# Kernel tuning notes

Hardware: AMD Instinct MI355X
Metric: run time of the kernel (lower is better)

The kernel has to match this reference:

```python
import jax, jax.numpy as jnp
import numpy as np

LEVELS = [(128, 128), (64, 64), (32, 32), (16, 16)]  # (h, w) per level
NUM_HEADS = 8
NUM_LEVELS = 4
NUM_POINTS = 4
EMBED_DIMS = 256


def _bilinear_sample(img, gx, gy):
    """grid_sample(mode='bilinear', padding_mode='zeros', align_corners=False).
    img: (B, H, W, C); gx, gy: (B, N) in [-1, 1]. Returns (B, N, C)."""
    B, H, W, C = img.shape
    x = ((gx + 1.0) * W - 1.0) * 0.5
    y = ((gy + 1.0) * H - 1.0) * 0.5
    x0 = jnp.floor(x)
    y0 = jnp.floor(y)
    wx1 = x - x0
    wy1 = y - y0
    flat = img.reshape(B, H * W, C)

    def gather(xf, yf, w):
        xi = xf.astype(jnp.int32)
        yi = yf.astype(jnp.int32)
        valid = (xi >= 0) & (xi < W) & (yi >= 0) & (yi < H)
        idx = jnp.clip(yi, 0, H - 1) * W + jnp.clip(xi, 0, W - 1)
        v = jnp.take_along_axis(flat, idx[..., None], axis=1)
        return v * (w * valid)[..., None]

    return (gather(x0, y0, (1 - wx1) * (1 - wy1))
            + gather(x0 + 1, y0, wx1 * (1 - wy1))
            + gather(x0, y0 + 1, (1 - wx1) * wy1)
            + gather(x0 + 1, y0 + 1, wx1 * wy1))


def _msda(value, sampling_locations, attention_weights):
    """value: (bs, nv, nh, dh); sampling_locations: (bs, nq, nh, L, P, 2);
    attention_weights: (bs, nq, nh, L, P). Returns (bs, nq, nh*dh)."""
    bs, nv, nh, dh = value.shape
    nq = sampling_locations.shape[1]
    P = sampling_locations.shape[4]
    grids = 2.0 * sampling_locations - 1.0
    out = jnp.zeros((bs * nh, nq, dh), value.dtype)
    start = 0
    for l, (h, w) in enumerate(LEVELS):
        v = value[:, start:start + h * w]                      # (bs, h*w, nh, dh)
        start += h * w
        v = v.transpose(0, 2, 1, 3).reshape(bs * nh, h, w, dh)
        g = grids[:, :, :, l].transpose(0, 2, 1, 3, 4).reshape(bs * nh, nq * P, 2)
        s = _bilinear_sample(v, g[..., 0], g[..., 1]).reshape(bs * nh, nq, P, dh)
        wgt = attention_weights[:, :, :, l].transpose(0, 2, 1, 3).reshape(bs * nh, nq, P)
        out = out + jnp.einsum('bqpd,bqp->bqd', s, wgt)
    return out.reshape(bs, nh, nq, dh).transpose(0, 2, 1, 3).reshape(bs, nq, nh * dh)


def setup_inputs() -> dict:
    key = jax.random.key(0)
    ks = jax.random.split(key, 12)
    bs, nq, D = 2, sum(h * w for h, w in LEVELS), EMBED_DIMS
    spatial_shapes = jnp.array(LEVELS, dtype=jnp.int32)
    starts = np.cumsum([0] + [h * w for h, w in LEVELS[:-1]])
    return {
        'query': jax.random.normal(ks[0], (bs, nq, D), jnp.float32),
        'value': jax.random.normal(ks[1], (bs, nq, D), jnp.float32),
        'reference_points': jax.random.uniform(ks[2], (bs, nq, NUM_LEVELS, 2), jnp.float32),
        'spatial_shapes': spatial_shapes,
        'level_start_index': jnp.asarray(starts, dtype=jnp.int32),
        'Wv': jax.random.normal(ks[3], (D, D), jnp.float32) * 0.02,
        'bv': jnp.zeros((D,), jnp.float32),
        'Wo': jax.random.normal(ks[4], (D, NUM_HEADS * NUM_LEVELS * NUM_POINTS * 2), jnp.float32) * 0.02,
        'bo': jax.random.normal(ks[5], (NUM_HEADS * NUM_LEVELS * NUM_POINTS * 2,), jnp.float32) * 0.5,
        'Wa': jax.random.normal(ks[6], (D, NUM_HEADS * NUM_LEVELS * NUM_POINTS), jnp.float32) * 0.02,
        'ba': jnp.zeros((NUM_HEADS * NUM_LEVELS * NUM_POINTS,), jnp.float32),
        'Wout': jax.random.normal(ks[7], (D, D), jnp.float32) * 0.02,
        'bout': jnp.zeros((D,), jnp.float32),
    }


def reference(query, value, reference_points, spatial_shapes, level_start_index,
              Wv, bv, Wo, bo, Wa, ba, Wout, bout):
    bs, nq, D = query.shape
    nv = value.shape[1]
    nh, L, P = NUM_HEADS, NUM_LEVELS, NUM_POINTS
    dh = D // nh
    identity = query

    v = (value @ Wv + bv).reshape(bs, nv, nh, dh)
    offs = (query @ Wo + bo).reshape(bs, nq, nh, L, P, 2)
    attw = jax.nn.softmax((query @ Wa + ba).reshape(bs, nq, nh, L * P), axis=-1)
    attw = attw.reshape(bs, nq, nh, L, P)

    # offset_normalizer = (w, h) per level
    norm = jnp.stack([spatial_shapes[:, 1], spatial_shapes[:, 0]], -1).astype(query.dtype)
    sampling_locations = (reference_points[:, :, None, :, None, :]
                          + offs / norm[None, None, None, :, None, :])

    out = _msda(v, sampling_locations, attw)
    out = out @ Wout + bout
    return out + identity  # dropout is identity in eval
```

## Files before the change

kernel.cpp:

```cpp
#include <hip/hip_runtime.h>

#define BS 2
#define NQ 21760
#define NV 21760
#define DIM 256
#define NH 8
#define DH 32
#define NL 4
#define NP 4

typedef __attribute__((ext_vector_type(8))) short bf16x8;
typedef __attribute__((ext_vector_type(4))) float f32x4;

__device__ __forceinline__ float bf2f(unsigned short s) {
    return __uint_as_float(((unsigned int)s) << 16);
}
__device__ __forceinline__ unsigned short f2bf(float f) {
    unsigned int u = __float_as_uint(f);
    u += 0x7fffu + ((u >> 16) & 1u);
    return (unsigned short)(u >> 16);
}

__global__ __launch_bounds__(64) void k_wprep(
    const float* __restrict__ Wo, const float* __restrict__ Wa,
    const float* __restrict__ Wv, const float* __restrict__ Wout,
    unsigned short* __restrict__ wsw)
{
    const int tile = blockIdx.x;
    const int lane = threadIdx.x;
    const float* W; int N, nb, kb;
    if (tile < 192) { nb = tile >> 3; kb = tile & 7;
        if (nb < 16) { W = Wo; N = 256; } else { W = Wa; N = 128; nb -= 16; } }
    else if (tile < 320) { int tt = tile - 192; nb = tt >> 3; kb = tt & 7; W = Wv;   N = 256; }
    else               { int tt = tile - 320; nb = tt >> 3; kb = tt & 7; W = Wout; N = 256; }
    const int quad = lane >> 4, l15 = lane & 15;
    const int col = nb * 16 + l15;
    unsigned int pk[4];
#pragma unroll
    for (int jj = 0; jj < 4; jj++) {
        int k0 = kb * 32 + quad * 8 + jj * 2;
        pk[jj] = (unsigned int)f2bf(W[(size_t)k0 * N + col])
               | ((unsigned int)f2bf(W[(size_t)(k0 + 1) * N + col]) << 16);
    }
    *(uint4*)(wsw + (size_t)tile * 512 + lane * 8) = *(const uint4*)pk;
}

__device__ __forceinline__ void stage_f32_512(const float* __restrict__ src,
                                              unsigned short* __restrict__ As)
{
    const int t = threadIdx.x;
    const int colg = t & 63;
    const int row0 = t >> 6;
#pragma unroll
    for (int i = 0; i < 8; i++) {
        int row = row0 + i * 8;
        float4 f = ((const float4*)(src + (size_t)row * 256))[colg];
        uint2 p;
        p.x = (unsigned int)f2bf(f.x) | ((unsigned int)f2bf(f.y) << 16);
        p.y = (unsigned int)f2bf(f.z) | ((unsigned int)f2bf(f.w) << 16);
        *(uint2*)&As[row * 264 + colg * 4] = p;
    }
}

__device__ __forceinline__ void stage_bf16_512(const unsigned short* __restrict__ src,
                                               unsigned short* __restrict__ As)
{
    const int t = threadIdx.x;
    const int colg = t & 63;
    const int row0 = t >> 6;
#pragma unroll
    for (int i = 0; i < 8; i++) {
        int row = row0 + i * 8;
        uint2 u = ((const uint2*)(src + (size_t)row * 256))[colg];
        *(uint2*)&As[row * 264 + colg * 4] = u;
    }
}

template<int NBH>
__device__ __forceinline__ void gemm_split2(const unsigned short* __restrict__ As,
                                            const unsigned short* __restrict__ wswb,
                                            f32x4* acc)
{
    const int t = threadIdx.x;
    const int w = t >> 6, lane = t & 63;
    const int wr = w & 1, wg = w >> 1;
    const int quad = lane >> 4, l15 = lane & 15;
    const int ra0 = (wr * 32 + l15) * 264;
#pragma unroll
    for (int kb = 0; kb < 8; kb++) {
        bf16x8 af0 = *(const bf16x8*)&As[ra0 + kb * 32 + quad * 8];
        bf16x8 af1 = *(const bf16x8*)&As[ra0 + 16 * 264 + kb * 32 + quad * 8];
#pragma unroll
        for (int nbi = 0; nbi < NBH; nbi++) {
            const int nb = wg * NBH + nbi;
            bf16x8 bf = *(const bf16x8*)(wswb + (((nb * 8 + kb) << 9) + (lane << 3)));
            acc[nbi]       = __builtin_amdgcn_mfma_f32_16x16x32_bf16(af0, bf, acc[nbi], 0, 0, 0);
            acc[NBH + nbi] = __builtin_amdgcn_mfma_f32_16x16x32_bf16(af1, bf, acc[NBH + nbi], 0, 0, 0);
        }
    }
}

__global__ __launch_bounds__(512) void k_proj(
    const float* __restrict__ value,
    const float* __restrict__ query,
    const float* __restrict__ refp,
    const unsigned short* __restrict__ wsw,
    const float* __restrict__ bv,
    const float* __restrict__ bo,
    const float* __restrict__ ba,
    unsigned short* __restrict__ v_hm,
    float* __restrict__ locs_ws,
    unsigned short* __restrict__ attw_b)
{
    __shared__ unsigned short As[64 * 264];
    const int t = threadIdx.x;
    const int w = t >> 6, lane = t & 63;
    const int wr = w & 1, wg = w >> 1;
    const int quad = lane >> 4, l15 = lane & 15;

    if (blockIdx.x < 680) {
        const size_t r0 = (size_t)blockIdx.x * 64;
        const int bb = (blockIdx.x >= 340);
        const int pix0 = (int)(r0 - (size_t)bb * NV);
        stage_f32_512(value + r0 * 256, As);
        __syncthreads();
        f32x4 acc[8];
#pragma unroll
        for (int i = 0; i < 8; i++) acc[i] = (f32x4){0.f, 0.f, 0.f, 0.f};
        gemm_split2<4>(As, wsw + 98304, acc);
#pragma unroll
        for (int rf = 0; rf < 2; rf++) {
#pragma unroll
            for (int nbi = 0; nbi < 4; nbi++) {
                const int col = (wg * 4 + nbi) * 16 + l15;
                const int h = col >> 5, ch = col & 31;
                const float bias = bv[col];
                const size_t hb = ((size_t)bb * NH + h) * NV;
#pragma unroll
                for (int r = 0; r < 4; r++) {
                    int pix = pix0 + wr * 32 + rf * 16 + quad * 4 + r;
                    v_hm[(hb + pix) * DH + ch] = f2bf(acc[rf * 4 + nbi][r] + bias);
                }
            }
        }
    } else {
        const size_t r0 = (size_t)(blockIdx.x - 680) * 64;
        stage_f32_512(query + r0 * 256, As);
        __syncthreads();
        f32x4 acc[12];
#pragma unroll
        for (int i = 0; i < 12; i++) acc[i] = (f32x4){0.f, 0.f, 0.f, 0.f};
        gemm_split2<6>(As, wsw, acc);
#pragma unroll
        for (int rf = 0; rf < 2; rf++) {
#pragma unroll
            for (int nbi = 0; nbi < 6; nbi++) {
                const int nb = wg * 6 + nbi;
                const int rowoff = wr * 32 + rf * 16 + quad * 4;
                if (nb < 16) {
                    const int col = nb * 16 + l15;
                    const int l = (col >> 3) & 3;
                    const int xy = col & 1;
                    const float rnorm = 1.f / (float)(128 >> l);
                    const float bo_c = bo[col];
#pragma unroll
                    for (int r = 0; r < 4; r++) {
                        size_t row = r0 + rowoff + r;
                        float ref = refp[row * 8 + l * 2 + xy];
                        locs_ws[row * 256 + col] = ref + (acc[rf * 6 + nbi][r] + bo_c) * rnorm;
                    }
                } else {
                    const int col = (nb - 16) * 16 + l15;
                    const float ba_c = ba[col];
#pragma unroll
                    for (int r = 0; r < 4; r++) {
                        float v = acc[rf * 6 + nbi][r] + ba_c;
                        float m = v;
                        m = fmaxf(m, __shfl_xor(m, 1, 64));
                        m = fmaxf(m, __shfl_xor(m, 2, 64));
                        m = fmaxf(m, __shfl_xor(m, 4, 64));
                        m = fmaxf(m, __shfl_xor(m, 8, 64));
                        float e = __expf(v - m);
                        float s = e;
                        s += __shfl_xor(s, 1, 64);
                        s += __shfl_xor(s, 2, 64);
                        s += __shfl_xor(s, 4, 64);
                        s += __shfl_xor(s, 8, 64);
                        size_t row = r0 + rowoff + r;
                        attw_b[row * 128 + col] = f2bf(e / s);
                    }
                }
            }
        }
    }
}

__global__ __launch_bounds__(256) void k_sample(
    const unsigned short* __restrict__ v_hm,
    const float* __restrict__ locs_ws,
    const unsigned short* __restrict__ attw_b,
    unsigned short* __restrict__ msda_ws)
{
    __shared__ uint2 tap[32 * 16 * 4];
    const int t = threadIdx.x;
    const int bid = blockIdx.x;

    const int xcd  = bid & 7;
    const int slot = bid >> 3;
    const int sub  = (slot >= 680) ? 1 : 0;
    const int chunk = slot - sub * 680;
    const int pair = xcd * 2 + sub;
    const int b = pair & 1;
    const int h = pair >> 1;
    const int q0 = chunk * 32;

#pragma unroll
    for (int i = 0; i < 2; i++) {
        const int tapid = t + i * 256;
        const int q  = tapid >> 4;
        const int tp = tapid & 15;
        const size_t row = (size_t)(b * NQ + q0 + q);
        float2 xy = *(const float2*)(locs_ws + row * 256 + h * 32 + tp * 2);
        float a   = bf2f(attw_b[row * 128 + h * 16 + tp]);

        const int l = tp >> 2;
        const int Wl = 128 >> l;
        const float Wf = (float)Wl;
        const int start = (l == 0) ? 0 : (l == 1) ? 16384 : (l == 2) ? 20480 : 21504;
        float x = xy.x * Wf - 0.5f;
        float y = xy.y * Wf - 0.5f;
        float xf = floorf(x), yf = floorf(y);
        int x0 = (int)xf, y0 = (int)yf;
        float wx1 = x - xf, wy1 = y - yf;
        float wx0 = 1.f - wx1, wy0 = 1.f - wy1;
#pragma unroll
        for (int c = 0; c < 4; c++) {
            const int dx = c & 1, dy = c >> 1;
            int xi = x0 + dx, yi = y0 + dy;
            bool valid = (xi >= 0) & (xi < Wl) & (yi >= 0) & (yi < Wl);
            int xc = min(max(xi, 0), Wl - 1);
            int yc = min(max(yi, 0), Wl - 1);
            float wc = valid ? a * (dx ? wx1 : wx0) * (dy ? wy1 : wy0) : 0.f;
            uint2 rec;
            rec.x = __float_as_uint(wc);
            rec.y = ((unsigned int)(start + yc * Wl + xc)) * 64u;
            tap[(tapid << 2) + c] = rec;
        }
    }
    __syncthreads();

    const int w      = t >> 6;
    const int lane   = t & 63;
    const int c4     = lane & 7;
    const int corner = (lane >> 3) & 3;
    const int tph    = lane >> 5;
    const unsigned int base =
        (unsigned int)((b * NH + h) * NV) * 64u + (unsigned int)c4 * 8u;
    const char* __restrict__ vb = (const char*)v_hm;

#pragma unroll 2
    for (int qq = 0; qq < 8; qq++) {
        const int q = w * 8 + qq;
        uint2 rec[8];
#pragma unroll
        for (int ti = 0; ti < 8; ti++)
            rec[ti] = tap[((q * 16 + ti * 2 + tph) << 2) + corner];
        uint2 dat[8];
#pragma unroll
        for (int ti = 0; ti < 8; ti++)
            dat[ti] = *(const uint2*)(vb + (base + rec[ti].y));
        float a0 = 0.f, a1 = 0.f, a2 = 0.f, a3 = 0.f;
#pragma unroll
        for (int ti = 0; ti < 8; ti++) {
            float wf = __uint_as_float(rec[ti].x);
            a0 = fmaf(wf, __uint_as_float(dat[ti].x << 16), a0);
            a1 = fmaf(wf, __uint_as_float(dat[ti].x & 0xffff0000u), a1);
            a2 = fmaf(wf, __uint_as_float(dat[ti].y << 16), a2);
            a3 = fmaf(wf, __uint_as_float(dat[ti].y & 0xffff0000u), a3);
        }
        a0 += __shfl_xor(a0, 8, 64);  a1 += __shfl_xor(a1, 8, 64);
        a2 += __shfl_xor(a2, 8, 64);  a3 += __shfl_xor(a3, 8, 64);
        a0 += __shfl_xor(a0, 16, 64); a1 += __shfl_xor(a1, 16, 64);
        a2 += __shfl_xor(a2, 16, 64); a3 += __shfl_xor(a3, 16, 64);
        a0 += __shfl_xor(a0, 32, 64); a1 += __shfl_xor(a1, 32, 64);
        a2 += __shfl_xor(a2, 32, 64); a3 += __shfl_xor(a3, 32, 64);
        if (lane < 8) {
            uint2 o;
            o.x = ((unsigned int)f2bf(a1) << 16) | (unsigned int)f2bf(a0);
            o.y = ((unsigned int)f2bf(a3) << 16) | (unsigned int)f2bf(a2);
            *(uint2*)(msda_ws + (size_t)(b * NQ + q0 + q) * DIM + h * DH + c4 * 4) = o;
        }
    }
}

__global__ __launch_bounds__(512) void k_out_mfma(
    const unsigned short* __restrict__ msda_ws,
    const unsigned short* __restrict__ wswo,
    const float* __restrict__ bout,
    const float* __restrict__ query,
    float* __restrict__ out)
{
    __shared__ unsigned short As[64 * 264];
    const size_t r0 = (size_t)blockIdx.x * 64;
    stage_bf16_512(msda_ws + r0 * 256, As);
    __syncthreads();

    f32x4 acc[8];
#pragma unroll
    for (int i = 0; i < 8; i++) acc[i] = (f32x4){0.f, 0.f, 0.f, 0.f};
    gemm_split2<4>(As, wswo, acc);

    const int t = threadIdx.x;
    const int w = t >> 6, lane = t & 63;
    const int wr = w & 1, wg = w >> 1;
    const int quad = lane >> 4, l15 = lane & 15;
#pragma unroll
    for (int rf = 0; rf < 2; rf++) {
#pragma unroll
        for (int nbi = 0; nbi < 4; nbi++) {
            const int col = (wg * 4 + nbi) * 16 + l15;
            const float bias = bout[col];
#pragma unroll
            for (int r = 0; r < 4; r++) {
                size_t row = r0 + wr * 32 + rf * 16 + quad * 4 + r;
                out[row * 256 + col] = acc[rf * 4 + nbi][r] + bias + query[row * 256 + col];
            }
        }
    }
}

extern "C" void kernel_launch(void* const* d_in, const int* in_sizes, int n_in,
                              void* d_out, int out_size, void* d_ws, size_t ws_size,
                              hipStream_t stream)
{
    const float* query = (const float*)d_in[0];
    const float* value = (const float*)d_in[1];
    const float* refp  = (const float*)d_in[2];
    const float* Wv   = (const float*)d_in[5];
    const float* bv   = (const float*)d_in[6];
    const float* Wo   = (const float*)d_in[7];
    const float* bo   = (const float*)d_in[8];
    const float* Wa   = (const float*)d_in[9];
    const float* ba   = (const float*)d_in[10];
    const float* Wout = (const float*)d_in[11];
    const float* bout = (const float*)d_in[12];
    float* out = (float*)d_out;

    char* ws = (char*)d_ws;
    unsigned short* v_hm = (unsigned short*)ws;    ws += (size_t)BS * NH * NV * DH * 2;
    float* locs_ws = (float*)ws;                   ws += (size_t)BS * NQ * DIM * 4;
    unsigned short* attw_b = (unsigned short*)ws;  ws += (size_t)BS * NQ * 128 * 2;
    unsigned short* msda_ws = (unsigned short*)ws; ws += (size_t)BS * NQ * DIM * 2;
    unsigned short* wsw = (unsigned short*)ws;

    k_wprep   <<<448, 64,  0, stream>>>(Wo, Wa, Wv, Wout, wsw);
    k_proj    <<<1360, 512, 0, stream>>>(value, query, refp, wsw, bv, bo, ba,
                                         v_hm, locs_ws, attw_b);
    k_sample  <<<10880, 256, 0, stream>>>(v_hm, locs_ws, attw_b, msda_ws);
    k_out_mfma<<<680, 512, 0, stream>>>(msda_ws, wsw + 163840, bout, query, out);
}
```

Before: 323.0 us.

## Switch to fp16, stage value stores through LDS, and restructure sampling per query

Replaces bf16 with fp16 throughout: weight prep, activation staging, the MFMA intrinsic and the sampling intermediates. The value projection now writes its tile into shared memory and then emits coalesced head-major rows, instead of scattering scalar stores. The sampling kernel gives each group of 8 lanes one query and accumulates all 64 taps serially, using a transposed tap table in LDS, which removes the cross-lane shuffle reduction. Fp16 changes rounding and range behaviour. The new sampling loop issues more dependent loads per lane and may expose gather latency differently.

```diff
diff --git a/kernel.cpp b/kernel.cpp
--- a/kernel.cpp
+++ b/kernel.cpp
@@ -1,4 +1,5 @@
 #include <hip/hip_runtime.h>
+#include <hip/hip_fp16.h>
 
 #define BS 2
 #define NQ 21760
@@ -9,16 +10,14 @@
 #define NL 4
 #define NP 4
 
-typedef __attribute__((ext_vector_type(8))) short bf16x8;
+typedef __attribute__((ext_vector_type(8))) _Float16 f16x8;
 typedef __attribute__((ext_vector_type(4))) float f32x4;
 
-__device__ __forceinline__ float bf2f(unsigned short s) {
-    return __uint_as_float(((unsigned int)s) << 16);
-}
-__device__ __forceinline__ unsigned short f2bf(float f) {
-    unsigned int u = __float_as_uint(f);
-    u += 0x7fffu + ((u >> 16) & 1u);
-    return (unsigned short)(u >> 16);
+__device__ __forceinline__ unsigned short f2h(float f) {
+    return __half_as_ushort(__float2half(f));
+}
+__device__ __forceinline__ float h2f(unsigned short s) {
+    return __half2float(__ushort_as_half(s));
 }
 
 __global__ __launch_bounds__(64) void k_wprep(
@@ -39,8 +38,8 @@
 #pragma unroll
     for (int jj = 0; jj < 4; jj++) {
         int k0 = kb * 32 + quad * 8 + jj * 2;
-        pk[jj] = (unsigned int)f2bf(W[(size_t)k0 * N + col])
-               | ((unsigned int)f2bf(W[(size_t)(k0 + 1) * N + col]) << 16);
+        pk[jj] = (unsigned int)f2h(W[(size_t)k0 * N + col])
+               | ((unsigned int)f2h(W[(size_t)(k0 + 1) * N + col]) << 16);
     }
     *(uint4*)(wsw + (size_t)tile * 512 + lane * 8) = *(const uint4*)pk;
 }
@@ -56,14 +55,14 @@
         int row = row0 + i * 8;
         float4 f = ((const float4*)(src + (size_t)row * 256))[colg];
         uint2 p;
-        p.x = (unsigned int)f2bf(f.x) | ((unsigned int)f2bf(f.y) << 16);
-        p.y = (unsigned int)f2bf(f.z) | ((unsigned int)f2bf(f.w) << 16);
+        p.x = (unsigned int)f2h(f.x) | ((unsigned int)f2h(f.y) << 16);
+        p.y = (unsigned int)f2h(f.z) | ((unsigned int)f2h(f.w) << 16);
         *(uint2*)&As[row * 264 + colg * 4] = p;
     }
 }
 
-__device__ __forceinline__ void stage_bf16_512(const unsigned short* __restrict__ src,
-                                               unsigned short* __restrict__ As)
+__device__ __forceinline__ void stage_h16_512(const unsigned short* __restrict__ src,
+                                              unsigned short* __restrict__ As)
 {
     const int t = threadIdx.x;
     const int colg = t & 63;
@@ -88,14 +87,14 @@
     const int ra0 = (wr * 32 + l15) * 264;
 #pragma unroll
     for (int kb = 0; kb < 8; kb++) {
-        bf16x8 af0 = *(const bf16x8*)&As[ra0 + kb * 32 + quad * 8];
-        bf16x8 af1 = *(const bf16x8*)&As[ra0 + 16 * 264 + kb * 32 + quad * 8];
+        f16x8 af0 = *(const f16x8*)&As[ra0 + kb * 32 + quad * 8];
+        f16x8 af1 = *(const f16x8*)&As[ra0 + 16 * 264 + kb * 32 + quad * 8];
 #pragma unroll
         for (int nbi = 0; nbi < NBH; nbi++) {
             const int nb = wg * NBH + nbi;
-            bf16x8 bf = *(const bf16x8*)(wswb + (((nb * 8 + kb) << 9) + (lane << 3)));
-            acc[nbi]       = __builtin_amdgcn_mfma_f32_16x16x32_bf16(af0, bf, acc[nbi], 0, 0, 0);
-            acc[NBH + nbi] = __builtin_amdgcn_mfma_f32_16x16x32_bf16(af1, bf, acc[NBH + nbi], 0, 0, 0);
+            f16x8 bf = *(const f16x8*)(wswb + (((nb * 8 + kb) << 9) + (lane << 3)));
+            acc[nbi]       = __builtin_amdgcn_mfma_f32_16x16x32_f16(af0, bf, acc[nbi], 0, 0, 0);
+            acc[NBH + nbi] = __builtin_amdgcn_mfma_f32_16x16x32_f16(af1, bf, acc[NBH + nbi], 0, 0, 0);
         }
     }
 }
@@ -128,20 +127,26 @@
 #pragma unroll
         for (int i = 0; i < 8; i++) acc[i] = (f32x4){0.f, 0.f, 0.f, 0.f};
         gemm_split2<4>(As, wsw + 98304, acc);
+        __syncthreads();
 #pragma unroll
         for (int rf = 0; rf < 2; rf++) {
 #pragma unroll
             for (int nbi = 0; nbi < 4; nbi++) {
                 const int col = (wg * 4 + nbi) * 16 + l15;
-                const int h = col >> 5, ch = col & 31;
                 const float bias = bv[col];
-                const size_t hb = ((size_t)bb * NH + h) * NV;
 #pragma unroll
                 for (int r = 0; r < 4; r++) {
-                    int pix = pix0 + wr * 32 + rf * 16 + quad * 4 + r;
-                    v_hm[(hb + pix) * DH + ch] = f2bf(acc[rf * 4 + nbi][r] + bias);
+                    int pixL = wr * 32 + rf * 16 + quad * 4 + r;
+                    As[pixL * 264 + col] = f2h(acc[rf * 4 + nbi][r] + bias);
                 }
             }
+        }
+        __syncthreads();
+        const int pix = t >> 3, c8 = t & 7;
+#pragma unroll
+        for (int hh = 0; hh < 8; hh++) {
+            uint2 d = *(const uint2*)&As[pix * 264 + hh * 32 + c8 * 4];
+            *(uint2*)(v_hm + (((size_t)bb * NH + hh) * NV + pix0 + pix) * DH + c8 * 4) = d;
         }
     } else {
         const size_t r0 = (size_t)(blockIdx.x - 680) * 64;
@@ -187,12 +192,23 @@
                         s += __shfl_xor(s, 4, 64);
                         s += __shfl_xor(s, 8, 64);
                         size_t row = r0 + rowoff + r;
-                        attw_b[row * 128 + col] = f2bf(e / s);
+                        attw_b[row * 128 + col] = f2h(e / s);
                     }
                 }
             }
         }
     }
+}
+
+__device__ __forceinline__ void acc4(float wf, uint2 d,
+                                     float& a0, float& a1, float& a2, float& a3)
+{
+    __half2 lo = *(__half2*)&d.x;
+    __half2 hi = *(__half2*)&d.y;
+    a0 = fmaf(wf, __half2float(__low2half(lo)),  a0);
+    a1 = fmaf(wf, __half2float(__high2half(lo)), a1);
+    a2 = fmaf(wf, __half2float(__low2half(hi)),  a2);
+    a3 = fmaf(wf, __half2float(__high2half(hi)), a3);
 }
 
 __global__ __launch_bounds__(256) void k_sample(
@@ -201,7 +217,7 @@
     const unsigned short* __restrict__ attw_b,
     unsigned short* __restrict__ msda_ws)
 {
-    __shared__ uint2 tap[32 * 16 * 4];
+    __shared__ uint2 tap[16 * 4 * 32];
     const int t = threadIdx.x;
     const int bid = blockIdx.x;
 
@@ -217,11 +233,11 @@
 #pragma unroll
     for (int i = 0; i < 2; i++) {
         const int tapid = t + i * 256;
-        const int q  = tapid >> 4;
-        const int tp = tapid & 15;
+        const int q  = tapid & 31;
+        const int tp = tapid >> 5;
         const size_t row = (size_t)(b * NQ + q0 + q);
         float2 xy = *(const float2*)(locs_ws + row * 256 + h * 32 + tp * 2);
-        float a   = bf2f(attw_b[row * 128 + h * 16 + tp]);
+        float a   = h2f(attw_b[row * 128 + h * 16 + tp]);
 
         const int l = tp >> 2;
         const int Wl = 128 >> l;
@@ -244,53 +260,40 @@
             uint2 rec;
             rec.x = __float_as_uint(wc);
             rec.y = ((unsigned int)(start + yc * Wl + xc)) * 64u;
-            tap[(tapid << 2) + c] = rec;
+            tap[(tp * 4 + c) * 32 + q] = rec;
         }
     }
     __syncthreads();
 
-    const int w      = t >> 6;
-    const int lane   = t & 63;
-    const int c4     = lane & 7;
-    const int corner = (lane >> 3) & 3;
-    const int tph    = lane >> 5;
-    const unsigned int base =
-        (unsigned int)((b * NH + h) * NV) * 64u + (unsigned int)c4 * 8u;
-    const char* __restrict__ vb = (const char*)v_hm;
-
-#pragma unroll 2
-    for (int qq = 0; qq < 8; qq++) {
-        const int q = w * 8 + qq;
-        uint2 rec[8];
-#pragma unroll
-        for (int ti = 0; ti < 8; ti++)
-            rec[ti] = tap[((q * 16 + ti * 2 + tph) << 2) + corner];
-        uint2 dat[8];
-#pragma unroll
-        for (int ti = 0; ti < 8; ti++)
-            dat[ti] = *(const uint2*)(vb + (base + rec[ti].y));
-        float a0 = 0.f, a1 = 0.f, a2 = 0.f, a3 = 0.f;
-#pragma unroll
-        for (int ti = 0; ti < 8; ti++) {
-            float wf = __uint_as_float(rec[ti].x);
-            a0 = fmaf(wf, __uint_as_float(dat[ti].x << 16), a0);
-            a1 = fmaf(wf, __uint_as_float(dat[ti].x & 0xffff0000u), a1);
-            a2 = fmaf(wf, __uint_as_float(dat[ti].y << 16), a2);
-            a3 = fmaf(wf, __uint_as_float(dat[ti].y & 0xffff0000u), a3);
-        }
-        a0 += __shfl_xor(a0, 8, 64);  a1 += __shfl_xor(a1, 8, 64);
-        a2 += __shfl_xor(a2, 8, 64);  a3 += __shfl_xor(a3, 8, 64);
-        a0 += __shfl_xor(a0, 16, 64); a1 += __shfl_xor(a1, 16, 64);
-        a2 += __shfl_xor(a2, 16, 64); a3 += __shfl_xor(a3, 16, 64);
-        a0 += __shfl_xor(a0, 32, 64); a1 += __shfl_xor(a1, 32, 64);
-        a2 += __shfl_xor(a2, 32, 64); a3 += __shfl_xor(a3, 32, 64);
-        if (lane < 8) {
-            uint2 o;
-            o.x = ((unsigned int)f2bf(a1) << 16) | (unsigned int)f2bf(a0);
-            o.y = ((unsigned int)f2bf(a3) << 16) | (unsigned int)f2bf(a2);
-            *(uint2*)(msda_ws + (size_t)(b * NQ + q0 + q) * DIM + h * DH + c4 * 4) = o;
-        }
-    }
+    const int w4   = t >> 6;
+    const int lane = t & 63;
+    const int ql   = lane >> 3;
+    const int c4   = lane & 7;
+    const int q    = w4 * 8 + ql;
+    const unsigned int c4off = (unsigned int)c4 * 8u;
+    const char* __restrict__ vb =
+        (const char*)(v_hm + (size_t)(b * NH + h) * NV * DH);
+
+    float a0 = 0.f, a1 = 0.f, a2 = 0.f, a3 = 0.f;
+#pragma unroll
+    for (int ti = 0; ti < 16; ti++) {
+        uint2 r0 = tap[(ti * 4 + 0) * 32 + q];
+        uint2 r1 = tap[(ti * 4 + 1) * 32 + q];
+        uint2 r2 = tap[(ti * 4 + 2) * 32 + q];
+        uint2 r3 = tap[(ti * 4 + 3) * 32 + q];
+        uint2 d0 = *(const uint2*)(vb + (r0.y + c4off));
+        uint2 d1 = *(const uint2*)(vb + (r1.y + c4off));
+        uint2 d2 = *(const uint2*)(vb + (r2.y + c4off));
+        uint2 d3 = *(const uint2*)(vb + (r3.y + c4off));
+        acc4(__uint_as_float(r0.x), d0, a0, a1, a2, a3);
+        acc4(__uint_as_float(r1.x), d1, a0, a1, a2, a3);
+        acc4(__uint_as_float(r2.x), d2, a0, a1, a2, a3);
+        acc4(__uint_as_float(r3.x), d3, a0, a1, a2, a3);
+    }
+    uint2 o;
+    o.x = (unsigned int)f2h(a0) | ((unsigned int)f2h(a1) << 16);
+    o.y = (unsigned int)f2h(a2) | ((unsigned int)f2h(a3) << 16);
+    *(uint2*)(msda_ws + (size_t)(b * NQ + q0 + q) * DIM + h * DH + c4 * 4) = o;
 }
 
 __global__ __launch_bounds__(512) void k_out_mfma(
@@ -302,7 +305,7 @@
 {
     __shared__ unsigned short As[64 * 264];
     const size_t r0 = (size_t)blockIdx.x * 64;
-    stage_bf16_512(msda_ws + r0 * 256, As);
+    stage_h16_512(msda_ws + r0 * 256, As);
     __syncthreads();
 
     f32x4 acc[8];
```

New measurement: 333.4 us. 3.2% more time.
